# Performance work log

Measured on AMD Instinct MI355X. Metric: run time of the kernel, lower is better.

The kernel has to match this reference:

```python
import jax, jax.numpy as jnp
import numpy as np

# dims
B, S, E = 32, 2048, 512          # batch, seq_length, emb_size
N, P, K = 256, 16, 16            # new_seq_len, sample_num, sub_seq_len
STRIDE = 8                       # ceil(S / N)
PAD = 4                          # ceil((STRIDE*(N-1) + K - S) / 2)


def setup_inputs() -> dict:
    key = jax.random.key(0)
    ks = jax.random.split(key, 6)
    return {
        "x": jax.random.normal(ks[0], (B, S, E), jnp.float32),
        "conv_w": jax.random.normal(ks[1], (E, E, K), jnp.float32) / np.float32(np.sqrt(E * K)),
        "conv_b": jax.random.normal(ks[2], (E,), jnp.float32) * 0.01,
        "lin_w": jax.random.normal(ks[3], (2, E), jnp.float32) / np.float32(np.sqrt(E)),
        "lin_b": jax.random.normal(ks[4], (2,), jnp.float32) * 0.01,
        "width_bias": jnp.asarray(0.5 * np.log(5.0 / 3.0), jnp.float32),  # log(sqrt(5/3))
    }


def reference(x, conv_w, conv_b, lin_w, lin_b, width_bias):
    # --- proj: Conv1d over sequence, [B,S,E] -> [B,N,E] ---
    xc = jnp.transpose(x, (0, 2, 1))  # [B,E,S]
    y = jax.lax.conv_general_dilated(
        xc, conv_w, (STRIDE,), [(PAD, PAD)],
        dimension_numbers=("NCH", "OIH", "NCH"),
    ) + conv_b[None, :, None]  # [B,E,N]
    y = jnp.transpose(y, (0, 2, 1))  # [B,N,E]

    # --- offset prediction: ReLU -> Linear(E, 2) ---
    off = jax.nn.relu(y) @ lin_w.T + lin_b  # [B,N,2]

    # --- SubSeqCoder.decode (weights = (1,1), width_bias added to last channel) ---
    anchor = (0.5 + jnp.arange(N, dtype=x.dtype)) / N  # [N]
    poi = 1.0 / N
    dx = jnp.tanh(off[:, :, 0]) * poi
    dw = jax.nn.relu(jnp.tanh(off[:, :, 1] + width_bias)) * poi
    x0 = jnp.clip(anchor[None, :] + dx - dw, 0.0, 1.0)  # box start, [B,N]
    x1 = jnp.clip(anchor[None, :] + dx + dw, 0.0, 1.0)  # box end

    # --- sample: linear interpolate (align_corners=True) from 2 -> P points ---
    t = jnp.linspace(0.0, 1.0, P, dtype=x.dtype)  # [P]
    gx = x0[:, :, None] * (1.0 - t) + x1[:, :, None] * t  # [B,N,P] in [0,1]

    # --- grid_sample nearest, padding_mode='border', align_corners=False ---
    gx = 2.0 * gx - 1.0  # normalized grid coord
    ix = ((gx + 1.0) * S - 1.0) * 0.5  # unnormalize (align_corners=False)
    idx = jnp.clip(jnp.round(ix).astype(jnp.int32), 0, S - 1)  # [B,N,P], round half-even matches nearbyint
    vals = jnp.take_along_axis(x, idx.reshape(B, N * P, 1), axis=1)  # [B,N*P,E]
    # output already in [B, N, P, E] layout (== torch permute(0,2,3,1))
    return vals.reshape(B, N, P, E)
```

## Files before the change

kernel.cpp:

```cpp
#include <hip/hip_runtime.h>
#include <cmath>

#define BATCH 32
#define SEQ   2048
#define EMB   512
#define NOUT  256
#define PS    16
#define KW    16
#define JTOT  8192
#define KCL   288

#define MB 64
#define NB 128
#define KS 32

__device__ __forceinline__ float xla_tanhf(float x) {
#pragma clang fp contract(off)
    float ax = fabsf(x);
    float xc = x;
    if (xc < -7.90531110763549805f) xc = -7.90531110763549805f;
    if (xc >  7.90531110763549805f) xc =  7.90531110763549805f;
    float x2 = xc * xc;
    float p = __builtin_fmaf(x2, -2.76076847742355e-16f, 2.00018790482477e-13f);
    p = __builtin_fmaf(x2, p, -8.60467152213735e-11f);
    p = __builtin_fmaf(x2, p,  5.12229709037114e-08f);
    p = __builtin_fmaf(x2, p,  1.48572235717979e-05f);
    p = __builtin_fmaf(x2, p,  6.37261928875436e-04f);
    p = __builtin_fmaf(x2, p,  4.89352455891786e-03f);
    float num = xc * p;
    float q = __builtin_fmaf(x2, 1.19825839466702e-06f, 1.18534705686654e-04f);
    q = __builtin_fmaf(x2, q, 2.26843463243900e-03f);
    q = __builtin_fmaf(x2, q, 4.89352518554385e-03f);
    float r = num / q;
    return (ax < 0.0004f) ? x : r;
}

__global__ __launch_bounds__(256) void k_transpose_w(const float* __restrict__ w,
                                                     float* __restrict__ wT) {
    int t = blockIdx.x * 256 + threadIdx.x;
    int o = t & 511;
    int i = (t >> 9) & 511;
    int k = t >> 18;
    wT[t] = w[(size_t)o * 8192 + i * 16 + k];
}

__global__ __launch_bounds__(256) void k_conv(const float* __restrict__ x,
                                              const float* __restrict__ wT,
                                              const float* __restrict__ cb,
                                              float* __restrict__ y) {
#pragma clang fp contract(off)
    __shared__ __align__(16) float sA[KS][MB + 4];
    __shared__ __align__(16) float sB[KS][NB];

    int bm  = blockIdx.x;
    int bn0 = bm << 6;
    int b   = bn0 >> 8;
    int n0  = bn0 & 255;
    int o0  = blockIdx.y << 7;

    int tid = threadIdx.x;
    int tm  = tid & 15;
    int tn  = tid >> 4;

    float ys[4][8], pk[4][8];
#pragma unroll
    for (int mi = 0; mi < 4; ++mi)
#pragma unroll
        for (int ni = 0; ni < 8; ++ni) { ys[mi][ni] = 0.0f; pk[mi][ni] = 0.0f; }

    const float* xb = x + (size_t)b * SEQ * EMB;

    for (int js = 0; js < 256; ++js) {
        int k  = js >> 4;
        int i0 = (js & 15) << 5;
        __syncthreads();
#pragma unroll
        for (int r = 0; r < 2; ++r) {
            int q  = tid + (r << 8);
            int m  = q >> 3;
            int c4 = (q & 7) << 2;
            int s  = ((n0 + m) << 3) - 4 + k;
            float4 v = make_float4(0.f, 0.f, 0.f, 0.f);
            if (s >= 0 && s < SEQ)
                v = *(const float4*)(xb + ((size_t)s << 9) + i0 + c4);
            sA[c4 + 0][m] = v.x; sA[c4 + 1][m] = v.y;
            sA[c4 + 2][m] = v.z; sA[c4 + 3][m] = v.w;
        }
        {
            const float* wrow = wT + (((size_t)js << 5) << 9) + o0;
#pragma unroll
            for (int r = 0; r < 4; ++r) {
                int q  = tid + (r << 8);
                int kk = q >> 5;
                int o4 = (q & 31) << 2;
                *(float4*)&sB[kk][o4] = *(const float4*)(wrow + ((size_t)kk << 9) + o4);
            }
        }
        __syncthreads();
#pragma unroll
        for (int kk = 0; kk < KS; ++kk) {
            float4 a  = *(const float4*)&sA[kk][tm << 2];
            float4 b0 = *(const float4*)&sB[kk][tn << 3];
            float4 b1 = *(const float4*)&sB[kk][(tn << 3) + 4];
            float av[4] = {a.x, a.y, a.z, a.w};
            float bv[8] = {b0.x, b0.y, b0.z, b0.w, b1.x, b1.y, b1.z, b1.w};
#pragma unroll
            for (int mi = 0; mi < 4; ++mi)
#pragma unroll
                for (int ni = 0; ni < 8; ++ni)
                    pk[mi][ni] = __builtin_fmaf(av[mi], bv[ni], pk[mi][ni]);
        }
        if ((js % 9) == 8 || js == 255) {
#pragma unroll
            for (int mi = 0; mi < 4; ++mi)
#pragma unroll
                for (int ni = 0; ni < 8; ++ni) {
                    ys[mi][ni] = ys[mi][ni] + pk[mi][ni];
                    pk[mi][ni] = 0.0f;
                }
        }
    }

    const float* cbp = cb + o0 + (tn << 3);
#pragma unroll
    for (int mi = 0; mi < 4; ++mi) {
        int n = n0 + (tm << 2) + mi;
        float* dst = y + (((size_t)(b << 8) + n) << 9) + o0 + (tn << 3);
#pragma unroll
        for (int ni = 0; ni < 8; ++ni)
            dst[ni] = ys[mi][ni] + cbp[ni];
    }
}

__global__ __launch_bounds__(256) void k_decode(const float* __restrict__ y,
                                               const float* __restrict__ lw,
                                               const float* __restrict__ lb,
                                               const float* __restrict__ wb,
                                               int* __restrict__ idx) {
#pragma clang fp contract(off)
    int bn = blockIdx.x * 256 + threadIdx.x;
    if (bn >= BATCH * NOUT) return;
    const float* yy = y + ((size_t)bn << 9);

    float s0, s1;
    {
        float p0 = 0.0f, p1 = 0.0f;
        for (int e = 0; e < KCL; ++e) {
            float v = yy[e];
            float r = v > 0.0f ? v : 0.0f;
            p0 = __builtin_fmaf(r, lw[e],       p0);
            p1 = __builtin_fmaf(r, lw[EMB + e], p1);
        }
        s0 = p0; s1 = p1;
    }
    {
        float p0 = 0.0f, p1 = 0.0f;
        for (int e = KCL; e < EMB; ++e) {
            float v = yy[e];
            float r = v > 0.0f ? v : 0.0f;
            p0 = __builtin_fmaf(r, lw[e],       p0);
            p1 = __builtin_fmaf(r, lw[EMB + e], p1);
        }
        s0 = s0 + p0; s1 = s1 + p1;
    }
    float off0 = s0 + lb[0];
    float off1 = s1 + lb[1];

    int n = bn & (NOUT - 1);
    float anchor = (0.5f + (float)n) / 256.0f;
    float dx  = xla_tanhf(off0) * 0.00390625f;
    float a1  = off1 + wb[0];
    float tww = xla_tanhf(a1);
    float rwv = tww > 0.0f ? tww : 0.0f;
    float dwv = rwv * 0.00390625f;
    float adx = anchor + dx;
    float x0 = adx - dwv; x0 = x0 < 0.0f ? 0.0f : (x0 > 1.0f ? 1.0f : x0);
    float x1 = adx + dwv; x1 = x1 < 0.0f ? 0.0f : (x1 > 1.0f ? 1.0f : x1);

    const float delta = 1.0f / 15.0f;
#pragma unroll
    for (int p = 0; p < PS; ++p) {
        float t  = (float)p * delta;
        float om = 1.0f - t;
        float gs = x0 * om + x1 * t;
        float gxn = 2.0f * gs - 1.0f;
        float gp1 = gxn + 1.0f;
        float ixx = (gp1 * 2048.0f - 1.0f) * 0.5f;
        float rr = rintf(ixx);
        int id = (int)rr;
        id = id < 0 ? 0 : (id > SEQ - 1 ? SEQ - 1 : id);
        idx[bn * PS + p] = id;
    }
}

__global__ __launch_bounds__(128) void k_gather(const float* __restrict__ x,
                                                const int* __restrict__ idx,
                                                float* __restrict__ out) {
    int g = blockIdx.x;
    int b = g >> 12;
    int sidx = idx[g];
    const float4* src = (const float4*)(x + (((size_t)b * SEQ + sidx) << 9));
    float4* dst = (float4*)(out + ((size_t)g << 9));
    dst[threadIdx.x] = src[threadIdx.x];
}

extern "C" void kernel_launch(void* const* d_in, const int* in_sizes, int n_in,
                              void* d_out, int out_size, void* d_ws, size_t ws_size,
                              hipStream_t stream) {
    const float* x      = (const float*)d_in[0];
    const float* conv_w = (const float*)d_in[1];
    const float* conv_b = (const float*)d_in[2];
    const float* lin_w  = (const float*)d_in[3];
    const float* lin_b  = (const float*)d_in[4];
    const float* wbias  = (const float*)d_in[5];
    float* out = (float*)d_out;

    float* wT  = (float*)d_out;
    float* y   = (float*)((char*)d_out + (size_t)16777216);
    int*   idx = (int*)d_ws;

    hipLaunchKernelGGL(k_transpose_w, dim3(16384), dim3(256), 0, stream, conv_w, wT);
    hipLaunchKernelGGL(k_conv,        dim3(128, 4), dim3(256), 0, stream, x, wT, conv_b, y);
    hipLaunchKernelGGL(k_decode,      dim3(32),    dim3(256), 0, stream, y, lin_w, lin_b, wbias, idx);
    hipLaunchKernelGGL(k_gather,      dim3(BATCH * NOUT * PS), dim3(128), 0, stream, x, idx, out);
}
```

Baseline: 1.007 ms.

## Double-buffer conv GEMM shared tiles and enlarge per-thread tile to 8x8

The conv GEMM kernel now uses double-buffered shared memory, prefetching the next K-slice into registers while computing the current one. The M tile also grows from 64 to 128, so each thread computes an 8x8 output block instead of 4x8. This is meant to hide global load latency and raise arithmetic intensity per shared-memory read. In exchange, the grid shrinks to 256 blocks, which can underfill the GPU's compute units, and register pressure rises, which may cut occupancy.

New measurement: 1.341 ms. 33.1% more time.

```diff
diff --git a/kernel.cpp b/kernel.cpp
--- a/kernel.cpp
+++ b/kernel.cpp
@@ -10,8 +10,8 @@
 #define JTOT  8192
 #define KCL   288
 
-#define MB 64
-#define NB 128
+#define MT 128
+#define NT 128
 #define KS 32
 
 __device__ __forceinline__ float xla_tanhf(float x) {
@@ -49,11 +49,10 @@
                                               const float* __restrict__ cb,
                                               float* __restrict__ y) {
 #pragma clang fp contract(off)
-    __shared__ __align__(16) float sA[KS][MB + 4];
-    __shared__ __align__(16) float sB[KS][NB];
-
-    int bm  = blockIdx.x;
-    int bn0 = bm << 6;
+    __shared__ __align__(16) float sA[2][KS][MT + 4];
+    __shared__ __align__(16) float sB[2][KS][NT];
+
+    int bn0 = blockIdx.x << 7;
     int b   = bn0 >> 8;
     int n0  = bn0 & 255;
     int o0  = blockIdx.y << 7;
@@ -62,74 +61,111 @@
     int tm  = tid & 15;
     int tn  = tid >> 4;
 
-    float ys[4][8], pk[4][8];
-#pragma unroll
-    for (int mi = 0; mi < 4; ++mi)
+    int ma  = tid & 127;
+    int kkq = tid >> 7;
+
+    float ys[8][8], pk[8][8];
+#pragma unroll
+    for (int mi = 0; mi < 8; ++mi)
 #pragma unroll
         for (int ni = 0; ni < 8; ++ni) { ys[mi][ni] = 0.0f; pk[mi][ni] = 0.0f; }
 
     const float* xb = x + (size_t)b * SEQ * EMB;
 
+    float4 ra[4], rb[4];
+
+#define LOAD_T(js_)                                                            \
+    {                                                                          \
+        int k_  = (js_) >> 4;                                                  \
+        int i0_ = ((js_) & 15) << 5;                                           \
+        int s_  = ((n0 + ma) << 3) - 4 + k_;                                   \
+        _Pragma("unroll")                                                      \
+        for (int r = 0; r < 4; ++r) {                                          \
+            int kk0 = (kkq << 4) + (r << 2);                                   \
+            ra[r] = make_float4(0.f, 0.f, 0.f, 0.f);                           \
+            if (s_ >= 0 && s_ < SEQ)                                           \
+                ra[r] = *(const float4*)(xb + ((size_t)s_ << 9) + i0_ + kk0);  \
+        }                                                                      \
+        const float* wrow_ = wT + (((size_t)(js_) << 5) << 9) + o0;            \
+        _Pragma("unroll")                                                      \
+        for (int r = 0; r < 4; ++r) {                                          \
+            int e  = (tid + (r << 8)) << 2;                                    \
+            int kk = e >> 7;                                                   \
+            int o4 = e & 127;                                                  \
+            rb[r] = *(const float4*)(wrow_ + ((size_t)kk << 9) + o4);          \
+        }                                                                      \
+    }
+
+#define WRITE_T(bf_)                                                           \
+    {                                                                          \
+        _Pragma("unroll")                                                      \
+        for (int r = 0; r < 4; ++r) {                                          \
+            int kk0 = (kkq << 4) + (r << 2);                                   \
+            sA[bf_][kk0 + 0][ma] = ra[r].x;                                    \
+            sA[bf_][kk0 + 1][ma] = ra[r].y;                                    \
+            sA[bf_][kk0 + 2][ma] = ra[r].z;                                    \
+            sA[bf_][kk0 + 3][ma] = ra[r].w;                                    \
+        }                                                                      \
+        _Pragma("unroll")                                                      \
+        for (int r = 0; r < 4; ++r) {                                          \
+            int e  = (tid + (r << 8)) << 2;                                    \
+            int kk = e >> 7;                                                   \
+            int o4 = e & 127;                                                  \
+            *(float4*)&sB[bf_][kk][o4] = rb[r];                                \
+        }                                                                      \
+    }
+
+    LOAD_T(0);
+    WRITE_T(0);
+    __syncthreads();
+
     for (int js = 0; js < 256; ++js) {
-        int k  = js >> 4;
-        int i0 = (js & 15) << 5;
-        __syncthreads();
-#pragma unroll
-        for (int r = 0; r < 2; ++r) {
-            int q  = tid + (r << 8);
-            int m  = q >> 3;
-            int c4 = (q & 7) << 2;
-            int s  = ((n0 + m) << 3) - 4 + k;
-            float4 v = make_float4(0.f, 0.f, 0.f, 0.f);
-            if (s >= 0 && s < SEQ)
-                v = *(const float4*)(xb + ((size_t)s << 9) + i0 + c4);
-            sA[c4 + 0][m] = v.x; sA[c4 + 1][m] = v.y;
-            sA[c4 + 2][m] = v.z; sA[c4 + 3][m] = v.w;
-        }
-        {
-            const float* wrow = wT + (((size_t)js << 5) << 9) + o0;
-#pragma unroll
-            for (int r = 0; r < 4; ++r) {
-                int q  = tid + (r << 8);
-                int kk = q >> 5;
-                int o4 = (q & 31) << 2;
-                *(float4*)&sB[kk][o4] = *(const float4*)(wrow + ((size_t)kk << 9) + o4);
-            }
-        }
-        __syncthreads();
+        int cur = js & 1;
+        if (js < 255) LOAD_T(js + 1);
+
 #pragma unroll
         for (int kk = 0; kk < KS; ++kk) {
-            float4 a  = *(const float4*)&sA[kk][tm << 2];
-            float4 b0 = *(const float4*)&sB[kk][tn << 3];
-            float4 b1 = *(const float4*)&sB[kk][(tn << 3) + 4];
-            float av[4] = {a.x, a.y, a.z, a.w};
+            float4 a0 = *(const float4*)&sA[cur][kk][tm << 2];
+            float4 a1 = *(const float4*)&sA[cur][kk][64 + (tm << 2)];
+            float4 b0 = *(const float4*)&sB[cur][kk][tn << 2];
+            float4 b1 = *(const float4*)&sB[cur][kk][64 + (tn << 2)];
+            float av[8] = {a0.x, a0.y, a0.z, a0.w, a1.x, a1.y, a1.z, a1.w};
             float bv[8] = {b0.x, b0.y, b0.z, b0.w, b1.x, b1.y, b1.z, b1.w};
 #pragma unroll
-            for (int mi = 0; mi < 4; ++mi)
+            for (int mi = 0; mi < 8; ++mi)
 #pragma unroll
                 for (int ni = 0; ni < 8; ++ni)
                     pk[mi][ni] = __builtin_fmaf(av[mi], bv[ni], pk[mi][ni]);
         }
         if ((js % 9) == 8 || js == 255) {
 #pragma unroll
-            for (int mi = 0; mi < 4; ++mi)
+            for (int mi = 0; mi < 8; ++mi)
 #pragma unroll
                 for (int ni = 0; ni < 8; ++ni) {
                     ys[mi][ni] = ys[mi][ni] + pk[mi][ni];
                     pk[mi][ni] = 0.0f;
                 }
         }
-    }
-
-    const float* cbp = cb + o0 + (tn << 3);
-#pragma unroll
-    for (int mi = 0; mi < 4; ++mi) {
-        int n = n0 + (tm << 2) + mi;
-        float* dst = y + (((size_t)(b << 8) + n) << 9) + o0 + (tn << 3);
-#pragma unroll
-        for (int ni = 0; ni < 8; ++ni)
-            dst[ni] = ys[mi][ni] + cbp[ni];
-    }
+        __syncthreads();
+        if (js < 255) {
+            WRITE_T(cur ^ 1);
+            __syncthreads();
+        }
+    }
+
+#pragma unroll
+    for (int mi = 0; mi < 8; ++mi) {
+        int m = (mi < 4) ? ((tm << 2) + mi) : (64 + (tm << 2) + mi - 4);
+        int n = n0 + m;
+        float* dst = y + (((size_t)(b << 8) + n) << 9) + o0;
+#pragma unroll
+        for (int ni = 0; ni < 8; ++ni) {
+            int oo = (ni < 4) ? ((tn << 2) + ni) : (64 + (tn << 2) + ni - 4);
+            dst[oo] = ys[mi][ni] + cb[o0 + oo];
+        }
+    }
+#undef LOAD_T
+#undef WRITE_T
 }
 
 __global__ __launch_bounds__(256) void k_decode(const float* __restrict__ y,
@@ -220,7 +256,7 @@
     int*   idx = (int*)d_ws;
 
     hipLaunchKernelGGL(k_transpose_w, dim3(16384), dim3(256), 0, stream, conv_w, wT);
-    hipLaunchKernelGGL(k_conv,        dim3(128, 4), dim3(256), 0, stream, x, wT, conv_b, y);
+    hipLaunchKernelGGL(k_conv,        dim3(64, 4), dim3(256), 0, stream, x, wT, conv_b, y);
     hipLaunchKernelGGL(k_decode,      dim3(32),    dim3(256), 0, stream, y, lin_w, lin_b, wbias, idx);
     hipLaunchKernelGGL(k_gather,      dim3(BATCH * NOUT * PS), dim3(128), 0, stream, x, idx, out);
 }
```

## Double-buffer conv GEMM shared-memory tiles with register prefetch

Applied to the files above, without the earlier changes.

The conv GEMM kernel now keeps two shared-memory tile buffers. The global loads for the next K-slice go into registers before the current slice's FMA loop runs, and are written to the other buffer afterwards. This hides global load latency behind compute and drops one barrier per iteration. In exchange it uses twice the LDS and more registers, which may lower occupancy on a grid of only 512 blocks.

After: 1.082 ms. 1.07x slower.

```diff
diff --git a/kernel.cpp b/kernel.cpp
--- a/kernel.cpp
+++ b/kernel.cpp
@@ -49,8 +49,8 @@
                                               const float* __restrict__ cb,
                                               float* __restrict__ y) {
 #pragma clang fp contract(off)
-    __shared__ __align__(16) float sA[KS][MB + 4];
-    __shared__ __align__(16) float sB[KS][NB];
+    __shared__ __align__(16) float sA[2][KS][MB + 4];
+    __shared__ __align__(16) float sB[2][KS][NB];
 
     int bm  = blockIdx.x;
     int bn0 = bm << 6;
@@ -70,38 +70,66 @@
 
     const float* xb = x + (size_t)b * SEQ * EMB;
 
+    float4 ra[2], rb[4];
+
+#define LOAD_T(js_)                                                            \
+    {                                                                          \
+        int k_  = (js_) >> 4;                                                  \
+        int i0_ = ((js_) & 15) << 5;                                           \
+        _Pragma("unroll")                                                      \
+        for (int r = 0; r < 2; ++r) {                                          \
+            int q  = tid + (r << 8);                                           \
+            int m  = q >> 3;                                                   \
+            int c4 = (q & 7) << 2;                                             \
+            int s  = ((n0 + m) << 3) - 4 + k_;                                 \
+            ra[r] = make_float4(0.f, 0.f, 0.f, 0.f);                           \
+            if (s >= 0 && s < SEQ)                                             \
+                ra[r] = *(const float4*)(xb + ((size_t)s << 9) + i0_ + c4);    \
+        }                                                                      \
+        const float* wrow_ = wT + (((size_t)(js_) << 5) << 9) + o0;            \
+        _Pragma("unroll")                                                      \
+        for (int r = 0; r < 4; ++r) {                                          \
+            int q  = tid + (r << 8);                                           \
+            int kk = q >> 5;                                                   \
+            int o4 = (q & 31) << 2;                                            \
+            rb[r] = *(const float4*)(wrow_ + ((size_t)kk << 9) + o4);          \
+        }                                                                      \
+    }
+
+#define WRITE_T(bf_)                                                           \
+    {                                                                          \
+        _Pragma("unroll")                                                      \
+        for (int r = 0; r < 2; ++r) {                                          \
+            int q  = tid + (r << 8);                                           \
+            int m  = q >> 3;                                                   \
+            int c4 = (q & 7) << 2;                                             \
+            sA[bf_][c4 + 0][m] = ra[r].x;                                      \
+            sA[bf_][c4 + 1][m] = ra[r].y;                                      \
+            sA[bf_][c4 + 2][m] = ra[r].z;                                      \
+            sA[bf_][c4 + 3][m] = ra[r].w;                                      \
+        }                                                                      \
+        _Pragma("unroll")                                                      \
+        for (int r = 0; r < 4; ++r) {                                          \
+            int q  = tid + (r << 8);                                           \
+            int kk = q >> 5;                                                   \
+            int o4 = (q & 31) << 2;                                            \
+            *(float4*)&sB[bf_][kk][o4] = rb[r];                                \
+        }                                                                      \
+    }
+
+    LOAD_T(0);
+    WRITE_T(0);
+    __syncthreads();
+
     for (int js = 0; js < 256; ++js) {
-        int k  = js >> 4;
-        int i0 = (js & 15) << 5;
-        __syncthreads();
-#pragma unroll
-        for (int r = 0; r < 2; ++r) {
-            int q  = tid + (r << 8);
-            int m  = q >> 3;
-            int c4 = (q & 7) << 2;
-            int s  = ((n0 + m) << 3) - 4 + k;
-            float4 v = make_float4(0.f, 0.f, 0.f, 0.f);
-            if (s >= 0 && s < SEQ)
-                v = *(const float4*)(xb + ((size_t)s << 9) + i0 + c4);
-            sA[c4 + 0][m] = v.x; sA[c4 + 1][m] = v.y;
-            sA[c4 + 2][m] = v.z; sA[c4 + 3][m] = v.w;
-        }
-        {
-            const float* wrow = wT + (((size_t)js << 5) << 9) + o0;
-#pragma unroll
-            for (int r = 0; r < 4; ++r) {
-                int q  = tid + (r << 8);
-                int kk = q >> 5;
-                int o4 = (q & 31) << 2;
-                *(float4*)&sB[kk][o4] = *(const float4*)(wrow + ((size_t)kk << 9) + o4);
-            }
-        }
-        __syncthreads();
+        int cur = js & 1;
+        if (js < 255) LOAD_T(js + 1);
+
 #pragma unroll
         for (int kk = 0; kk < KS; ++kk) {
-            float4 a  = *(const float4*)&sA[kk][tm << 2];
-            float4 b0 = *(const float4*)&sB[kk][tn << 3];
-            float4 b1 = *(const float4*)&sB[kk][(tn << 3) + 4];
+            float4 a  = *(const float4*)&sA[cur][kk][tm << 2];
+            float4 b0 = *(const float4*)&sB[cur][kk][tn << 3];
+            float4 b1 = *(const float4*)&sB[cur][kk][(tn << 3) + 4];
             float av[4] = {a.x, a.y, a.z, a.w};
             float bv[8] = {b0.x, b0.y, b0.z, b0.w, b1.x, b1.y, b1.z, b1.w};
 #pragma unroll
@@ -119,6 +147,8 @@
                     pk[mi][ni] = 0.0f;
                 }
         }
+        if (js < 255) WRITE_T(cur ^ 1);
+        __syncthreads();
     }
 
     const float* cbp = cb + o0 + (tn << 3);
@@ -130,6 +160,8 @@
         for (int ni = 0; ni < 8; ++ni)
             dst[ni] = ys[mi][ni] + cbp[ni];
     }
+#undef LOAD_T
+#undef WRITE_T
 }
 
 __global__ __launch_bounds__(256) void k_decode(const float* __restrict__ y,
```
